# Kernel tuning notes

Hardware: AMD Instinct MI355X
Metric: run time of the kernel (lower is better)

The kernel has to match this reference:

```python
import jax, jax.numpy as jnp
import numpy as np

NUM_USERS = 100000
NUM_ITEMS = 50000
N_NODES = NUM_USERS + NUM_ITEMS
D = 64
N_LAYERS = 3
E = 2000000
B = 1024
ALPHA_PREF = 1.0


def setup_inputs() -> dict:
    key = jax.random.key(0)
    k1, k2, k3, k4 = jax.random.split(key, 4)
    embed = jax.random.normal(k1, (N_NODES, D), dtype=jnp.float32) * 0.1
    edge_index = jax.random.randint(k2, (2, E), 0, N_NODES, dtype=jnp.int32)
    users = jax.random.randint(k3, (B,), 0, NUM_USERS, dtype=jnp.int32)
    items = jax.random.randint(k4, (B,), 0, NUM_ITEMS, dtype=jnp.int32)
    return {"embed": embed, "edge_index": edge_index, "users": users, "items": items}


def _lightgcn_propagate(x, row, col, norm):
    # message: norm * x[row] (x_j = source), aggregated (add) at col (target)
    msg = norm[:, None] * x[row]                      # [E, D]
    return jnp.zeros_like(x).at[col].add(msg)         # [N, D]


def reference(embed, edge_index, users, items):
    row, col = edge_index[0], edge_index[1]
    n = embed.shape[0]
    # degree normalization (depends only on edge_index; same every layer)
    deg = jnp.zeros((n,), jnp.float32).at[row].add(1.0)
    deg_inv = jnp.clip(deg, 1.0, None) ** -0.5
    norm = deg_inv[row] * deg_inv[col]                # [E]

    x = embed
    for _ in range(N_LAYERS):
        x = _lightgcn_propagate(x, row, col, norm)

    u_emb = x[users]                                  # [B, D]
    i_emb = x[items + NUM_USERS]                      # [B, D]

    # mask = (row == users[:,None]) flattened selection of col; edge e is
    # selected once per batch element b with users[b] == row[e] -> multiplicity
    cnt = jnp.zeros((n,), jnp.float32).at[users].add(1.0)
    mult = cnt[row]                                   # [E] selection multiplicity

    # PreferenceShapley surrogate: softmax over selected neighbor embeddings
    # of alpha_pref * <neigh_emb, mean(u_emb)>, flattened over the batch.
    context = u_emb.mean(0)                           # [D]
    neigh = x[col]                                    # [E, D]
    logits = ALPHA_PREF * (neigh @ context)           # [E]
    masked = jnp.where(mult > 0, logits, -jnp.inf)
    mx = jnp.max(masked)
    ew = mult * jnp.exp(logits - mx)                  # [E] weighted exp (0 where unselected)
    z = jnp.clip(ew.sum(), 1e-12, None)
    neigh_aggr = (ew[:, None] * neigh).sum(0) / z     # [D]

    score = (u_emb * i_emb).sum(-1) + u_emb @ neigh_aggr  # [B]
    return jax.nn.sigmoid(score)
```

## Files before the change

kernel.cpp:

```cpp
#include <hip/hip_runtime.h>
#include <float.h>
#include <math.h>

#define NUM_USERS 100000
#define NUM_ITEMS 50000
#define NNODES    150000
#define DIM       64
#define NEDGE     2000000
#define BATCH     1024
#define SEL_CAP   (1 << 18)
#define LOGIT_BLOCKS 512

#define SLICES   1024
#define EPS      1956
#define NBUK     293
#define BCAP     8192
#define SCAP     16
#define OVF_CAP  4096

__device__ __forceinline__ float wave_sum64(float v) {
    #pragma unroll
    for (int off = 32; off > 0; off >>= 1) v += __shfl_xor(v, off, 64);
    return v;
}

__device__ __forceinline__ float bf2f(unsigned short s) {
    return __uint_as_float(((unsigned int)s) << 16);
}
__device__ __forceinline__ unsigned short f2bf(float f) {
    unsigned int u = __float_as_uint(f);
    return (unsigned short)((u + 0x7fffu + ((u >> 16) & 1u)) >> 16);
}


__global__ __launch_bounds__(512) void sort_kernel(
        const int* __restrict__ row, const int* __restrict__ col,
        const int* __restrict__ ucnt,
        unsigned char* __restrict__ cntC8, unsigned char* __restrict__ cntR8,
        unsigned int* __restrict__ midC2, unsigned short* __restrict__ midR2,
        uint2* __restrict__ ovfC, unsigned int* __restrict__ ovfR,
        int* __restrict__ novfC_g, int* __restrict__ novfR_g,
        int* __restrict__ n_sel, int* __restrict__ sel_col, float* __restrict__ sel_w) {
    __shared__ unsigned int hc[NBUK], hr[NBUK];
    __shared__ unsigned int   stC[NBUK * SCAP];
    __shared__ unsigned short stR[NBUK * SCAP];
    __shared__ int lcnt, lbase;
    __shared__ int2 buf[256];
    int blk = blockIdx.x, t = threadIdx.x;
    for (int i = t; i < NBUK; i += 512) { hc[i] = 0; hr[i] = 0; }
    if (t == 0) lcnt = 0;
    __syncthreads();
    int e0 = blk * EPS;
    int e1 = e0 + EPS; if (e1 > NEDGE) e1 = NEDGE;
    for (int base = e0 + t * 4; base < e1; base += 2048) {
        if (base + 4 <= e1) {
            int4 r4 = *(const int4*)(row + base);
            int4 c4 = *(const int4*)(col + base);
            #pragma unroll
            for (int q = 0; q < 4; ++q) {
                int c = (q == 0) ? c4.x : (q == 1) ? c4.y : (q == 2) ? c4.z : c4.w;
                int r = (q == 0) ? r4.x : (q == 1) ? r4.y : (q == 2) ? r4.z : r4.w;
                int bc = c >> 9;
                unsigned int kc = atomicAdd(&hc[bc], 1u);
                unsigned int v = ((unsigned int)(c & 511) << 18) | (unsigned int)r;
                if (kc < SCAP) stC[bc * SCAP + kc] = v;
                else { int i = atomicAdd(novfC_g, 1); if (i < OVF_CAP) ovfC[i] = make_uint2((unsigned int)bc, v); }
                int br = r >> 9;
                unsigned int kr = atomicAdd(&hr[br], 1u);
                if (kr < SCAP) stR[br * SCAP + kr] = (unsigned short)(r & 511);
                else { int i = atomicAdd(novfR_g, 1); if (i < OVF_CAP) ovfR[i] = ((unsigned int)br << 9) | (unsigned int)(r & 511); }
                int u = ucnt[r];
                if (u > 0) { int i = atomicAdd(&lcnt, 1); if (i < 256) buf[i] = make_int2(c, u); }
            }
        } else {
            for (int e = base; e < e1; ++e) {
                int r = row[e], c = col[e];
                int bc = c >> 9;
                unsigned int kc = atomicAdd(&hc[bc], 1u);
                unsigned int v = ((unsigned int)(c & 511) << 18) | (unsigned int)r;
                if (kc < SCAP) stC[bc * SCAP + kc] = v;
                else { int i = atomicAdd(novfC_g, 1); if (i < OVF_CAP) ovfC[i] = make_uint2((unsigned int)bc, v); }
                int br = r >> 9;
                unsigned int kr = atomicAdd(&hr[br], 1u);
                if (kr < SCAP) stR[br * SCAP + kr] = (unsigned short)(r & 511);
                else { int i = atomicAdd(novfR_g, 1); if (i < OVF_CAP) ovfR[i] = ((unsigned int)br << 9) | (unsigned int)(r & 511); }
                int u = ucnt[r];
                if (u > 0) { int i = atomicAdd(&lcnt, 1); if (i < 256) buf[i] = make_int2(c, u); }
            }
        }
    }
    __syncthreads();
    for (int j = t; j < NBUK * SCAP; j += 512) {
        int b = j >> 4, k = j & (SCAP - 1);
        unsigned int cc = hc[b]; if (cc > SCAP) cc = SCAP;
        if ((unsigned int)k < cc)
            midC2[(size_t)b * (SLICES * SCAP) + blk * SCAP + k] = stC[j];
        unsigned int cr = hr[b]; if (cr > SCAP) cr = SCAP;
        if ((unsigned int)k < cr)
            midR2[(size_t)b * (SLICES * SCAP) + blk * SCAP + k] = stR[j];
    }
    if (t < NBUK) {
        unsigned int cc = hc[t]; if (cc > SCAP) cc = SCAP;
        unsigned int cr = hr[t]; if (cr > SCAP) cr = SCAP;
        cntC8[(size_t)blk * NBUK + t] = (unsigned char)cc;
        cntR8[(size_t)blk * NBUK + t] = (unsigned char)cr;
    }
    if (t == 0) {
        int c = lcnt; c = c < 256 ? c : 256;
        lbase = atomicAdd(n_sel, c);
    }
    __syncthreads();
    int c = lcnt; c = c < 256 ? c : 256;
    int b = lbase;
    for (int i = t; i < c; i += 512) {
        int o = b + i;
        if (o < SEL_CAP) { sel_col[o] = buf[i].x; sel_w[o] = (float)buf[i].y; }
    }
}


__global__ __launch_bounds__(1024) void bfinal_kernel(
        const unsigned int* __restrict__ midC2, const unsigned char* __restrict__ cntC8,
        const unsigned short* __restrict__ midR2, const unsigned char* __restrict__ cntR8,
        const uint2* __restrict__ ovfC, const unsigned int* __restrict__ ovfR,
        const int* __restrict__ novfC_g, const int* __restrict__ novfR_g,
        const float4* __restrict__ embed,
        int* __restrict__ rptr, int* __restrict__ rend, int* __restrict__ src_sorted,
        float* __restrict__ dinv, float* __restrict__ dinv2,
        uint2* __restrict__ y0) {
    __shared__ int cnt[512], sm[512], cur[512];
    __shared__ unsigned int stage[BCAP];
    __shared__ int nstage;
    __shared__ unsigned char lc[SLICES];
    __shared__ float dinvL[512];
    int bb = blockIdx.x, t = threadIdx.x;
    if (bb < NBUK) {
        int b = bb;
        if (t < SLICES) lc[t] = cntC8[(size_t)t * NBUK + b];
        if (t < 512) cnt[t] = 0;
        if (t == 0) nstage = 0;
        __syncthreads();
        size_t cbase = (size_t)b * (SLICES * SCAP);
        for (int j = t; j < SLICES * SCAP; j += 1024) {
            if ((unsigned int)(j & (SCAP - 1)) < (unsigned int)lc[j >> 4]) {
                unsigned int v = midC2[cbase + j];
                atomicAdd(&cnt[v >> 18], 1);
                int i = atomicAdd(&nstage, 1);
                if (i < BCAP) stage[i] = v;
            }
        }
        int noC = *novfC_g; if (noC > OVF_CAP) noC = OVF_CAP;
        for (int i = t; i < noC; i += 1024) {
            if ((int)ovfC[i].x == b) {
                unsigned int v = ovfC[i].y;
                atomicAdd(&cnt[v >> 18], 1);
                int k = atomicAdd(&nstage, 1);
                if (k < BCAP) stage[k] = v;
            }
        }
        __syncthreads();
        if (t < 512) sm[t] = cnt[t];
        __syncthreads();
        for (int off = 1; off < 512; off <<= 1) {
            int v = 0;
            if (t < 512 && t >= off) v = sm[t - off];
            __syncthreads();
            if (t < 512) sm[t] += v;
            __syncthreads();
        }
        int s0 = b * BCAP;
        if (t < 512) {
            int excl = s0 + sm[t] - cnt[t];
            int n = b * 512 + t;
            if (n < NNODES) { rptr[n] = excl; rend[n] = s0 + sm[t]; }
            cur[t] = excl;
        }
        __syncthreads();
        int ns = nstage; if (ns > BCAP) ns = BCAP;
        for (int j = t; j < ns; j += 1024) {
            unsigned int v = stage[j];
            int dst = atomicAdd(&cur[v >> 18], 1);
            src_sorted[dst] = (int)(v & 0x3FFFFu);
        }
    } else {
        int b = bb - NBUK;
        if (t < SLICES) lc[t] = cntR8[(size_t)t * NBUK + b];
        if (t < 512) cnt[t] = 0;
        __syncthreads();
        size_t cbase = (size_t)b * (SLICES * SCAP);
        for (int j = t; j < SLICES * SCAP; j += 1024) {
            if ((unsigned int)(j & (SCAP - 1)) < (unsigned int)lc[j >> 4])
                atomicAdd(&cnt[midR2[cbase + j]], 1);
        }
        int noR = *novfR_g; if (noR > OVF_CAP) noR = OVF_CAP;
        for (int i = t; i < noR; i += 1024) {
            unsigned int pv = ovfR[i];
            if ((int)(pv >> 9) == b) atomicAdd(&cnt[pv & 511u], 1);
        }
        if (b == 0 && t < 16) y0[(size_t)NNODES * 16 + t] = make_uint2(0u, 0u);
        __syncthreads();
        if (t < 512) {
            int n = b * 512 + t;
            if (n < NNODES) {
                float d = fmaxf((float)cnt[t], 1.0f);
                float di = rsqrtf(d);
                dinv[n] = di; dinv2[n] = 1.0f / d;
                dinvL[t] = di;
            }
        }
        __syncthreads();
        int nbase = b * 512;
        int nmax = NNODES - nbase; if (nmax > 512) nmax = 512;
        if (nmax < 0) nmax = 0;
        for (int i = t; i < nmax * 16; i += 1024) {
            int ln = i >> 4, slot = i & 15;
            float d = dinvL[ln];
            float4 v = embed[(size_t)(nbase + ln) * 16 + slot];
            unsigned int w0 = (unsigned int)f2bf(v.x * d) | ((unsigned int)f2bf(v.y * d) << 16);
            unsigned int w1 = (unsigned int)f2bf(v.z * d) | ((unsigned int)f2bf(v.w * d) << 16);
            y0[(size_t)(nbase + ln) * 16 + slot] = make_uint2(w0, w1);
        }
    }
}


#define ACC8(V) do { \
    a0 += __uint_as_float((V).x << 16); a1 += __uint_as_float((V).x & 0xffff0000u); \
    a2 += __uint_as_float((V).y << 16); a3 += __uint_as_float((V).y & 0xffff0000u); \
    a4 += __uint_as_float((V).z << 16); a5 += __uint_as_float((V).z & 0xffff0000u); \
    a6 += __uint_as_float((V).w << 16); a7 += __uint_as_float((V).w & 0xffff0000u); \
} while (0)

__device__ __forceinline__ void prop_node(
        const uint4* __restrict__ x_in, uint4* __restrict__ x_out,
        const int* __restrict__ ptr, const int* __restrict__ rend,
        const int* __restrict__ src,
        const float* __restrict__ scale, int node, int sl) {
    int i = ptr[node], e = rend[node];
    float sc = scale[node];
    float a0 = 0.f, a1 = 0.f, a2 = 0.f, a3 = 0.f;
    float a4 = 0.f, a5 = 0.f, a6 = 0.f, a7 = 0.f;
    int p0, p1, p2, p3;
    if (i + 4 <= e) { p0 = src[i]; p1 = src[i + 1]; p2 = src[i + 2]; p3 = src[i + 3]; }
    while (i + 8 <= e) {
        uint4 w0 = x_in[p0 * 8 + sl];
        uint4 w1 = x_in[p1 * 8 + sl];
        uint4 w2 = x_in[p2 * 8 + sl];
        uint4 w3 = x_in[p3 * 8 + sl];
        p0 = src[i + 4]; p1 = src[i + 5]; p2 = src[i + 6]; p3 = src[i + 7];
        i += 4;
        ACC8(w0); ACC8(w1); ACC8(w2); ACC8(w3);
    }
    if (i + 4 <= e) {
        uint4 w0 = x_in[p0 * 8 + sl];
        uint4 w1 = x_in[p1 * 8 + sl];
        uint4 w2 = x_in[p2 * 8 + sl];
        uint4 w3 = x_in[p3 * 8 + sl];
        i += 4;
        ACC8(w0); ACC8(w1); ACC8(w2); ACC8(w3);
    }
    if (i < e) {
        int q0 = src[i];
        int q1 = (i + 1 < e) ? src[i + 1] : NNODES;
        int q2 = (i + 2 < e) ? src[i + 2] : NNODES;
        uint4 w0 = x_in[q0 * 8 + sl];
        uint4 w1 = x_in[q1 * 8 + sl];
        uint4 w2 = x_in[q2 * 8 + sl];
        ACC8(w0); ACC8(w1); ACC8(w2);
    }
    uint4 o;
    o.x = (unsigned int)f2bf(a0 * sc) | ((unsigned int)f2bf(a1 * sc) << 16);
    o.y = (unsigned int)f2bf(a2 * sc) | ((unsigned int)f2bf(a3 * sc) << 16);
    o.z = (unsigned int)f2bf(a4 * sc) | ((unsigned int)f2bf(a5 * sc) << 16);
    o.w = (unsigned int)f2bf(a6 * sc) | ((unsigned int)f2bf(a7 * sc) << 16);
    x_out[(size_t)node * 8 + sl] = o;
}

__global__ __launch_bounds__(256, 8) void prop_kernel(
        const uint4* __restrict__ x_in, uint4* __restrict__ x_out,
        const int* __restrict__ ptr, const int* __restrict__ rend,
        const int* __restrict__ src,
        const float* __restrict__ scale) {
    int gid  = blockIdx.x * blockDim.x + threadIdx.x;
    int node = gid >> 3;
    int sl   = gid & 7;
    if (node > NNODES) return;
    if (node == NNODES) {
        x_out[(size_t)node * 8 + sl] = make_uint4(0u, 0u, 0u, 0u);
        return;
    }
    prop_node(x_in, x_out, ptr, rend, src, scale, node, sl);
}

__global__ __launch_bounds__(256, 8) void prop_list_kernel(
        const uint4* __restrict__ x_in, uint4* __restrict__ x_out,
        const int* __restrict__ ptr, const int* __restrict__ rend,
        const int* __restrict__ src,
        const float* __restrict__ scale,
        const int* __restrict__ users, const int* __restrict__ items,
        const int* __restrict__ sel_col, const int* __restrict__ n_sel_p) {
    int n = *n_sel_p; if (n > SEL_CAP) n = SEL_CAP;
    int total = (2 * BATCH + n) * 8;
    int nth = gridDim.x * blockDim.x;
    for (int gid = blockIdx.x * blockDim.x + threadIdx.x; gid < total; gid += nth) {
        int li = gid >> 3;
        int sl = gid & 7;
        int node;
        if (li < BATCH) {
            node = users[li];
        } else if (li < 2 * BATCH) {
            node = items[li - BATCH] + NUM_USERS;
        } else {
            node = sel_col[li - 2 * BATCH];
        }
        prop_node(x_in, x_out, ptr, rend, src, scale, node, sl);
    }
}


__global__ void ucnt_kernel(const int* __restrict__ users, int* __restrict__ ucnt) {
    int b = blockIdx.x * blockDim.x + threadIdx.x;
    if (b < BATCH) atomicAdd(&ucnt[users[b]], 1);
}

__global__ __launch_bounds__(256) void ctx_part_kernel(
        const unsigned short* __restrict__ x, const int* __restrict__ users,
        float* __restrict__ ctx) {
    __shared__ float sm[256];
    int lane = threadIdx.x & 63, wl = threadIdx.x >> 6;
    int b0 = blockIdx.x * 16 + wl * 4;
    float acc = 0.0f;
    #pragma unroll
    for (int k = 0; k < 4; ++k)
        acc += bf2f(x[users[b0 + k] * DIM + lane]);
    sm[threadIdx.x] = acc;
    __syncthreads();
    if (wl == 0)
        atomicAdd(&ctx[lane], sm[lane] + sm[64 + lane] + sm[128 + lane] + sm[192 + lane]);
}

__global__ void softmax_kernel(const unsigned short* __restrict__ x,
                               const float* __restrict__ ctx,
                               const int* __restrict__ sel_col,
                               const float* __restrict__ sel_w,
                               const int* __restrict__ n_sel_p,
                               float* __restrict__ S, float* __restrict__ zp) {
    __shared__ float smS[4 * 64];
    __shared__ float smZ[4];
    int lane = threadIdx.x & 63, wl = threadIdx.x >> 6;
    int n = *n_sel_p; if (n > SEL_CAP) n = SEL_CAP;
    float c = ctx[lane] * (1.0f / BATCH);
    float accS = 0.0f, accZ = 0.0f;
    int stride = gridDim.x * 4;
    for (int idx = blockIdx.x * 4 + wl; idx < n; idx += stride) {
        int node = sel_col[idx];
        float xv = bf2f(x[node * DIM + lane]);
        float v = wave_sum64(xv * c);
        float w = sel_w[idx] * __expf(v);
        accS = fmaf(w, xv, accS);
        accZ += w;
    }
    smS[wl * 64 + lane] = accS;
    if (lane == 0) smZ[wl] = accZ;
    __syncthreads();
    if (wl == 0) {
        float s = smS[lane] + smS[64 + lane] + smS[128 + lane] + smS[192 + lane];
        atomicAdd(&S[lane], s);
    }
    if (threadIdx.x == 0) atomicAdd(zp, smZ[0] + smZ[1] + smZ[2] + smZ[3]);
}

__global__ void score_kernel(const unsigned short* __restrict__ x, const int* __restrict__ users,
                             const int* __restrict__ items, const float* __restrict__ S,
                             const float* __restrict__ zp, float* __restrict__ out) {
    int gid = blockIdx.x * blockDim.x + threadIdx.x;
    int b = gid >> 6, lane = gid & 63;
    if (b >= BATCH) return;
    float z = fmaxf(*zp, 1e-12f);
    float na = S[lane] / z;
    int u = users[b], it = items[b] + NUM_USERS;
    float v = bf2f(x[u * DIM + lane]) * (bf2f(x[it * DIM + lane]) + na);
    v = wave_sum64(v);
    if (lane == 0) out[b] = 1.0f / (1.0f + __expf(-v));
}


extern "C" void kernel_launch(void* const* d_in, const int* in_sizes, int n_in,
                              void* d_out, int out_size, void* d_ws, size_t ws_size,
                              hipStream_t stream) {
    const float* embed = (const float*)d_in[0];
    const int*   edge  = (const int*)d_in[1];
    const int*   row   = edge;
    const int*   col   = edge + NEDGE;
    const int*   users = (const int*)d_in[2];
    const int*   items = (const int*)d_in[3];
    float*       out   = (float*)d_out;
    char*        ws    = (char*)d_ws;

    size_t off = 0;
    auto A = [&](size_t bytes) { size_t o = off; off += (bytes + 255) & ~(size_t)255; return o; };
    size_t o_midC2 = A((size_t)NBUK * SLICES * SCAP * 4);
    size_t o_midR2 = A((size_t)NBUK * SLICES * SCAP * 2);
    size_t o_xa    = A((size_t)(NNODES + 1) * DIM * 2);
    size_t o_xb    = A((size_t)(NNODES + 1) * DIM * 2);
    size_t o_src   = A((size_t)NBUK * BCAP * 4);
    size_t o_cntC8 = A((size_t)SLICES * NBUK);
    size_t o_cntR8 = A((size_t)SLICES * NBUK);
    size_t o_ovfC  = A((size_t)OVF_CAP * 8);
    size_t o_ovfR  = A((size_t)OVF_CAP * 4);
    size_t o_selc  = A((size_t)SEL_CAP * 4);
    size_t o_selw  = A((size_t)SEL_CAP * 4);
    size_t o_zero  = off;
    size_t o_ucnt  = A((size_t)NNODES * 4);
    size_t o_misc  = A(1024);
    size_t zero_bytes = off - o_zero;
    size_t o_dinv  = A((size_t)NNODES * 4);
    size_t o_dinv2 = A((size_t)NNODES * 4);
    size_t o_rptr  = A((size_t)NNODES * 4);
    size_t o_rend  = A((size_t)NNODES * 4);

    unsigned int*   midC2 = (unsigned int*)(ws + o_midC2);
    unsigned short* midR2 = (unsigned short*)(ws + o_midR2);
    unsigned short* xa   = (unsigned short*)(ws + o_xa);
    unsigned short* xb   = (unsigned short*)(ws + o_xb);
    int*   srcS  = (int*)(ws + o_src);
    unsigned char* cntC8 = (unsigned char*)(ws + o_cntC8);
    unsigned char* cntR8 = (unsigned char*)(ws + o_cntR8);
    uint2* ovfC  = (uint2*)(ws + o_ovfC);
    unsigned int* ovfR = (unsigned int*)(ws + o_ovfR);
    int*   selc  = (int*)(ws + o_selc);
    float* selw  = (float*)(ws + o_selw);
    int*   ucnt  = (int*)(ws + o_ucnt);
    int*   nsel  = (int*)(ws + o_misc);
    float* zp    = (float*)(ws + o_misc + 8);
    float* S     = (float*)(ws + o_misc + 256);
    float* ctx   = (float*)(ws + o_misc + 512);
    int*   novfC = (int*)(ws + o_misc + 768);
    int*   novfR = (int*)(ws + o_misc + 772);
    float* dinv  = (float*)(ws + o_dinv);
    float* dinv2 = (float*)(ws + o_dinv2);
    int*   rptr  = (int*)(ws + o_rptr);
    int*   rend  = (int*)(ws + o_rend);

    hipMemsetAsync(ws + o_zero, 0, zero_bytes, stream);

    ucnt_kernel<<<(BATCH + 255) / 256, 256, 0, stream>>>(users, ucnt);

    sort_kernel<<<SLICES, 512, 0, stream>>>(row, col, ucnt, cntC8, cntR8,
                                            midC2, midR2, ovfC, ovfR, novfC, novfR,
                                            nsel, selc, selw);
    bfinal_kernel<<<2 * NBUK, 1024, 0, stream>>>(midC2, cntC8, midR2, cntR8,
                                                 ovfC, ovfR, novfC, novfR,
                                                 (const float4*)embed, rptr, rend, srcS,
                                                 dinv, dinv2, (uint2*)xa);

    int prop_blocks = ((NNODES + 1) * 8 + 255) / 256;
    prop_kernel<<<prop_blocks, 256, 0, stream>>>((const uint4*)xa, (uint4*)xb, rptr, rend, srcS, dinv2);
    prop_kernel<<<prop_blocks, 256, 0, stream>>>((const uint4*)xb, (uint4*)xa, rptr, rend, srcS, dinv2);
    prop_list_kernel<<<1024, 256, 0, stream>>>((const uint4*)xa, (uint4*)xb,
                                               rptr, rend, srcS, dinv,
                                               users, items, selc, nsel);

    ctx_part_kernel<<<64, 256, 0, stream>>>(xb, users, ctx);
    softmax_kernel<<<LOGIT_BLOCKS, 256, 0, stream>>>(xb, ctx, selc, selw, nsel, S, zp);

    score_kernel<<<(BATCH * 64 + 255) / 256, 256, 0, stream>>>(xb, users, items, S, zp, out);
}
```

Measured before the change: 248.4 us.

## Replace CSR adjacency with fixed-capacity padded per-node neighbor lists

```diff
diff --git a/kernel.cpp b/kernel.cpp
--- a/kernel.cpp
+++ b/kernel.cpp
@@ -14,8 +14,8 @@
 #define SLICES   1024
 #define EPS      1956
 #define NBUK     293
-#define BCAP     8192
 #define SCAP     16
+#define NCAP     48
 #define OVF_CAP  4096
 
 __device__ __forceinline__ float wave_sum64(float v) {
@@ -125,12 +125,10 @@
         const uint2* __restrict__ ovfC, const unsigned int* __restrict__ ovfR,
         const int* __restrict__ novfC_g, const int* __restrict__ novfR_g,
         const float4* __restrict__ embed,
-        int* __restrict__ rptr, int* __restrict__ rend, int* __restrict__ src_sorted,
+        int* __restrict__ rend, int* __restrict__ src_sorted,
         float* __restrict__ dinv, float* __restrict__ dinv2,
         uint2* __restrict__ y0) {
-    __shared__ int cnt[512], sm[512], cur[512];
-    __shared__ unsigned int stage[BCAP];
-    __shared__ int nstage;
+    __shared__ int cnt[512];
     __shared__ unsigned char lc[SLICES];
     __shared__ float dinvL[512];
     int bb = blockIdx.x, t = threadIdx.x;
@@ -138,49 +136,35 @@
         int b = bb;
         if (t < SLICES) lc[t] = cntC8[(size_t)t * NBUK + b];
         if (t < 512) cnt[t] = 0;
-        if (t == 0) nstage = 0;
         __syncthreads();
         size_t cbase = (size_t)b * (SLICES * SCAP);
+        int nb0 = b * 512;
         for (int j = t; j < SLICES * SCAP; j += 1024) {
             if ((unsigned int)(j & (SCAP - 1)) < (unsigned int)lc[j >> 4]) {
                 unsigned int v = midC2[cbase + j];
-                atomicAdd(&cnt[v >> 18], 1);
-                int i = atomicAdd(&nstage, 1);
-                if (i < BCAP) stage[i] = v;
+                int node = (int)(v >> 18);
+                int k = atomicAdd(&cnt[node], 1);
+                if (k < NCAP)
+                    src_sorted[(size_t)(nb0 + node) * NCAP + k] = (int)(v & 0x3FFFFu);
             }
         }
         int noC = *novfC_g; if (noC > OVF_CAP) noC = OVF_CAP;
         for (int i = t; i < noC; i += 1024) {
             if ((int)ovfC[i].x == b) {
                 unsigned int v = ovfC[i].y;
-                atomicAdd(&cnt[v >> 18], 1);
-                int k = atomicAdd(&nstage, 1);
-                if (k < BCAP) stage[k] = v;
+                int node = (int)(v >> 18);
+                int k = atomicAdd(&cnt[node], 1);
+                if (k < NCAP)
+                    src_sorted[(size_t)(nb0 + node) * NCAP + k] = (int)(v & 0x3FFFFu);
             }
         }
         __syncthreads();
-        if (t < 512) sm[t] = cnt[t];
-        __syncthreads();
-        for (int off = 1; off < 512; off <<= 1) {
-            int v = 0;
-            if (t < 512 && t >= off) v = sm[t - off];
-            __syncthreads();
-            if (t < 512) sm[t] += v;
-            __syncthreads();
-        }
-        int s0 = b * BCAP;
         if (t < 512) {
-            int excl = s0 + sm[t] - cnt[t];
-            int n = b * 512 + t;
-            if (n < NNODES) { rptr[n] = excl; rend[n] = s0 + sm[t]; }
-            cur[t] = excl;
-        }
-        __syncthreads();
-        int ns = nstage; if (ns > BCAP) ns = BCAP;
-        for (int j = t; j < ns; j += 1024) {
-            unsigned int v = stage[j];
-            int dst = atomicAdd(&cur[v >> 18], 1);
-            src_sorted[dst] = (int)(v & 0x3FFFFu);
+            int n = nb0 + t;
+            if (n < NNODES) {
+                int c = cnt[t]; if (c > NCAP) c = NCAP;
+                rend[n] = n * NCAP + c;
+            }
         }
     } else {
         int b = bb - NBUK;
@@ -233,10 +217,10 @@
 
 __device__ __forceinline__ void prop_node(
         const uint4* __restrict__ x_in, uint4* __restrict__ x_out,
-        const int* __restrict__ ptr, const int* __restrict__ rend,
+        const int* __restrict__ rend,
         const int* __restrict__ src,
         const float* __restrict__ scale, int node, int sl) {
-    int i = ptr[node], e = rend[node];
+    int i = node * NCAP, e = rend[node];
     float sc = scale[node];
     float a0 = 0.f, a1 = 0.f, a2 = 0.f, a3 = 0.f;
     float a4 = 0.f, a5 = 0.f, a6 = 0.f, a7 = 0.f;
@@ -278,7 +262,7 @@
 
 __global__ __launch_bounds__(256, 8) void prop_kernel(
         const uint4* __restrict__ x_in, uint4* __restrict__ x_out,
-        const int* __restrict__ ptr, const int* __restrict__ rend,
+        const int* __restrict__ rend,
         const int* __restrict__ src,
         const float* __restrict__ scale) {
     int gid  = blockIdx.x * blockDim.x + threadIdx.x;
@@ -289,12 +273,12 @@
         x_out[(size_t)node * 8 + sl] = make_uint4(0u, 0u, 0u, 0u);
         return;
     }
-    prop_node(x_in, x_out, ptr, rend, src, scale, node, sl);
+    prop_node(x_in, x_out, rend, src, scale, node, sl);
 }
 
 __global__ __launch_bounds__(256, 8) void prop_list_kernel(
         const uint4* __restrict__ x_in, uint4* __restrict__ x_out,
-        const int* __restrict__ ptr, const int* __restrict__ rend,
+        const int* __restrict__ rend,
         const int* __restrict__ src,
         const float* __restrict__ scale,
         const int* __restrict__ users, const int* __restrict__ items,
@@ -313,7 +297,7 @@
         } else {
             node = sel_col[li - 2 * BATCH];
         }
-        prop_node(x_in, x_out, ptr, rend, src, scale, node, sl);
+        prop_node(x_in, x_out, rend, src, scale, node, sl);
     }
 }
 
@@ -403,7 +387,7 @@
     size_t o_midR2 = A((size_t)NBUK * SLICES * SCAP * 2);
     size_t o_xa    = A((size_t)(NNODES + 1) * DIM * 2);
     size_t o_xb    = A((size_t)(NNODES + 1) * DIM * 2);
-    size_t o_src   = A((size_t)NBUK * BCAP * 4);
+    size_t o_src   = A((size_t)NNODES * NCAP * 4);
     size_t o_cntC8 = A((size_t)SLICES * NBUK);
     size_t o_cntR8 = A((size_t)SLICES * NBUK);
     size_t o_ovfC  = A((size_t)OVF_CAP * 8);
@@ -416,7 +400,6 @@
     size_t zero_bytes = off - o_zero;
     size_t o_dinv  = A((size_t)NNODES * 4);
     size_t o_dinv2 = A((size_t)NNODES * 4);
-    size_t o_rptr  = A((size_t)NNODES * 4);
     size_t o_rend  = A((size_t)NNODES * 4);
 
     unsigned int*   midC2 = (unsigned int*)(ws + o_midC2);
@@ -439,7 +422,6 @@
     int*   novfR = (int*)(ws + o_misc + 772);
     float* dinv  = (float*)(ws + o_dinv);
     float* dinv2 = (float*)(ws + o_dinv2);
-    int*   rptr  = (int*)(ws + o_rptr);
     int*   rend  = (int*)(ws + o_rend);
 
     hipMemsetAsync(ws + o_zero, 0, zero_bytes, stream);
@@ -451,14 +433,14 @@
                                             nsel, selc, selw);
     bfinal_kernel<<<2 * NBUK, 1024, 0, stream>>>(midC2, cntC8, midR2, cntR8,
                                                  ovfC, ovfR, novfC, novfR,
-                                                 (const float4*)embed, rptr, rend, srcS,
+                                                 (const float4*)embed, rend, srcS,
                                                  dinv, dinv2, (uint2*)xa);
 
     int prop_blocks = ((NNODES + 1) * 8 + 255) / 256;
-    prop_kernel<<<prop_blocks, 256, 0, stream>>>((const uint4*)xa, (uint4*)xb, rptr, rend, srcS, dinv2);
-    prop_kernel<<<prop_blocks, 256, 0, stream>>>((const uint4*)xb, (uint4*)xa, rptr, rend, srcS, dinv2);
+    prop_kernel<<<prop_blocks, 256, 0, stream>>>((const uint4*)xa, (uint4*)xb, rend, srcS, dinv2);
+    prop_kernel<<<prop_blocks, 256, 0, stream>>>((const uint4*)xb, (uint4*)xa, rend, srcS, dinv2);
     prop_list_kernel<<<1024, 256, 0, stream>>>((const uint4*)xa, (uint4*)xb,
-                                               rptr, rend, srcS, dinv,
+                                               rend, srcS, dinv,
                                                users, items, selc, nsel);
 
     ctx_part_kernel<<<64, 256, 0, stream>>>(xb, users, ctx);
```

Result: slower. 255.9 us (+3.0%).
